# Performance work log

Measured on AMD Instinct MI355X. Metric: run time of the kernel, lower is better.

Reference implementation:

```python
import jax, jax.numpy as jnp
import numpy as np

N_NODES = 15
K = 5
L_IN = 1920
C_OUT = 256
L3 = L_IN - 3 * K + 3  # 1908
EPS = 1e-5


def setup_inputs() -> dict:
    key = jax.random.key(0)
    ks = jax.random.split(key, 18)
    B, E = 128, 56
    s = 0.05
    inp = {
        'X': jax.random.normal(ks[0], (B, N_NODES, L_IN), jnp.float32),
        'edge_index': jax.random.randint(ks[1], (2, E), 0, N_NODES),
        'edge_weight': jax.random.uniform(ks[2], (E,), jnp.float32),
        # grouped conv params (groups = N_NODES): per-group channels 1->16->32->1
        'conv1_w': jax.random.normal(ks[3], (16 * N_NODES, 1, K), jnp.float32) * s,
        'conv1_b': jnp.zeros((16 * N_NODES,), jnp.float32),
        'conv2_w': jax.random.normal(ks[4], (32 * N_NODES, 16, K), jnp.float32) * s,
        'conv2_b': jnp.zeros((32 * N_NODES,), jnp.float32),
        'conv3_w': jax.random.normal(ks[5], (N_NODES, 32, K), jnp.float32) * s,
        'conv3_b': jnp.zeros((N_NODES,), jnp.float32),
        # GCNConv: lin weight [out,in] + bias
        'gcn_w': jax.random.normal(ks[6], (C_OUT, L3), jnp.float32) * s,
        'gcn_b': jnp.zeros((C_OUT,), jnp.float32),
        'lin1_w': jax.random.normal(ks[7], (C_OUT, L_IN), jnp.float32) * s,
        'lin1_b': jnp.zeros((C_OUT,), jnp.float32),
        # GraphNorm params
        'gn_w': jnp.ones((C_OUT,), jnp.float32),
        'gn_b': jnp.zeros((C_OUT,), jnp.float32),
        'gn_ms': jnp.ones((C_OUT,), jnp.float32),
        'out_w': jax.random.normal(ks[8], (16, C_OUT), jnp.float32) * s,
        'out_b': jnp.zeros((16,), jnp.float32),
    }
    return inp


def _gconv(x, w, b):
    # grouped valid conv1d, NCH layout
    y = jax.lax.conv_general_dilated(
        x, w, window_strides=(1,), padding='VALID',
        dimension_numbers=('NCH', 'OIH', 'NCH'),
        feature_group_count=N_NODES)
    return y + b[None, :, None]


def _gcn(x, edge_index, edge_weight, W, b):
    # x: [B, N, L3]; batched GCNConv with shared edge structure (no per-t loop)
    src, dst = edge_index[0], edge_index[1]
    loop = jnp.arange(N_NODES)
    src = jnp.concatenate([src, loop])
    dst = jnp.concatenate([dst, loop])
    ew = jnp.concatenate([edge_weight, jnp.ones((N_NODES,), edge_weight.dtype)])
    deg = jnp.zeros((N_NODES,), ew.dtype).at[dst].add(ew)  # in-degree on target
    dinv = jnp.where(deg > 0, jax.lax.rsqrt(deg), 0.0)
    norm = dinv[src] * ew * dinv[dst]  # [E']
    xl = jnp.einsum('bnf,of->bno', x, W)  # [B, N, C_OUT]
    msg = norm[None, :, None] * xl[:, src, :]  # [B, E', C_OUT]
    out = jnp.zeros_like(xl).at[:, dst, :].add(msg)
    return out + b


def reference(X, edge_index, edge_weight, conv1_w, conv1_b, conv2_w, conv2_b,
              conv3_w, conv3_b, gcn_w, gcn_b, lin1_w, lin1_b, gn_w, gn_b,
              gn_ms, out_w, out_b):
    h = jax.nn.leaky_relu(_gconv(X, conv1_w, conv1_b), 0.01)
    h = jax.nn.leaky_relu(_gconv(h, conv2_w, conv2_b), 0.01)
    h = jax.nn.leaky_relu(_gconv(h, conv3_w, conv3_b), 0.01)  # [B, N, L3]
    T = _gcn(h, edge_index, edge_weight, gcn_w, gcn_b)  # [B, N, C_OUT]
    # GraphNorm with batch=None -> single graph over dim 0
    mean = T.mean(axis=0, keepdims=True)
    out = T - mean * gn_ms
    var = (out * out).mean(axis=0, keepdims=True)
    T = gn_w * out / jnp.sqrt(var + EPS) + gn_b
    T = jax.nn.elu(T + jnp.einsum('bnl,ol->bno', X, lin1_w) + lin1_b)
    output = T.mean(axis=1)  # global_mean_pool over nodes -> [B, C_OUT]
    class_output = output @ out_w.T + out_b  # [B, 16]
    return (output, class_output)
```

## Files before the change

kernel.cpp:

```cpp
#include <hip/hip_runtime.h>

typedef unsigned short u16;
typedef unsigned int   u32;

typedef short shortx8   __attribute__((ext_vector_type(8)));
typedef float floatx4   __attribute__((ext_vector_type(4)));
typedef float floatx16  __attribute__((ext_vector_type(16)));
typedef u32   uintx4    __attribute__((ext_vector_type(4)));

typedef u32     u32a     __attribute__((may_alias));
typedef uintx4  uintx4a  __attribute__((may_alias));
typedef shortx8 shortx8a __attribute__((may_alias));

__device__ __forceinline__ u16 f2bf(float f){
  union { float f; u32 i; } v; v.f = f;
  return (u16)((v.i + 0x7fffu + ((v.i >> 16) & 1u)) >> 16);
}
__device__ __forceinline__ u16 f2bf_fast(float f){
  union { float f; u32 i; } v; v.f = f;
  return (u16)((v.i + 0x8000u) >> 16);
}
__device__ __forceinline__ u32 pack2(float lo, float hi){
  union { float f; u32 i; } a, b; a.f = lo; b.f = hi;
  return __builtin_amdgcn_perm(b.i + 0x8000u, a.i + 0x8000u, 0x07060302u);
}
__device__ __forceinline__ u32 cvtpk2(float lo, float hi){
#if __has_builtin(__builtin_amdgcn_cvt_pk_bf16_f32)
  auto pv = __builtin_amdgcn_cvt_pk_bf16_f32(lo, hi);
  if constexpr (sizeof(pv) == 4){
    u32 out; __builtin_memcpy(&out, &pv, 4); return out;
  } else {
    return pack2(lo, hi);
  }
#else
  return pack2(lo, hi);
#endif
}
__device__ __forceinline__ float lrelu(float v){ return fmaxf(v, 0.01f*v); }

__global__ void __launch_bounds__(256, 4) fused_conv(
    const float* __restrict__ X,
    const float* __restrict__ w1, const float* __restrict__ b1,
    const float* __restrict__ w2, const float* __restrict__ b2,
    const float* __restrict__ w3, const float* __restrict__ b3,
    u16* __restrict__ h3p, u16* __restrict__ Xb,
    const float* __restrict__ lw, u16* __restrict__ lwb,
    const float* __restrict__ gw, u16* __restrict__ gwp){
  const int tid  = threadIdx.x;
  const int node = blockIdx.z;
  const int p0   = blockIdx.x * 120;
  const int b0   = blockIdx.y * 8;

  __shared__ __attribute__((aligned(16))) u16 sH1[2*1632];
  __shared__ __attribute__((aligned(16))) u16 sH2[2*2720];
  __shared__ __attribute__((aligned(16))) u16 sW2f[2560];
  __shared__ __attribute__((aligned(16))) u16 sW3f[160];
  __shared__ u16 sXb[8*136];
  __shared__ float sW1[80], sB1[16], sB2[32];

  {
    const int bid = blockIdx.x + 16*(blockIdx.y + 16*blockIdx.z);
    int gid = bid*256 + tid;
    if (gid < 491520){
      lwb[gid] = f2bf(lw[gid]);
    } else {
      int g2 = gid - 491520;
      int row = g2 / 1920;
      int col = g2 - row*1920;
      gwp[g2] = (col < 1908) ? f2bf(gw[row*1908 + col]) : (u16)0;
    }
  }

  {
    const int bls = tid >> 5, i0 = tid & 31;
    const float* xrow = X  + (size_t)((b0 + bls)*15 + node)*1920;
    u16*        xbrow = Xb + (size_t)((b0 + bls)*15 + node)*1920;
    #pragma unroll
    for (int u = 0; u < 5; ++u){
      int i = i0 + 32*u;
      if (i < 136){
        int g = p0 + i;
        float xv = (g < 1920) ? xrow[g] : 0.f;
        u16 xb = f2bf_fast(xv);
        sXb[bls*136 + i] = xb;
        if (i < 120) xbrow[g] = xb;
      }
    }
    #pragma unroll
    for (int u = 0; u < 10; ++u){
      int d = tid + 256*u;
      int j = d & 7, oc = (d >> 3) & 31, kh = (d >> 8) & 1, tap = d >> 9;
      sW2f[d] = f2bf(w2[node*2560 + (oc*16 + kh*8 + j)*5 + tap]);
    }
    if (tid < 160){
      int icc = tid / 5, tp = tid - 5*icc;
      sW3f[tp*32 + icc] = f2bf(w3[node*160 + tid]);
    }
    if (tid < 80) sW1[tid] = w1[node*80 + tid];
    if (tid < 16) sB1[tid] = b1[node*16 + tid];
    if (tid < 32) sB2[tid] = b2[node*32 + tid];
  }
  __syncthreads();

  const int w = tid >> 6, lane = tid & 63;
  const int pw = w >> 1, ph = w & 1;
  const int m = lane & 15, quad = lane >> 4;
  const int t32 = lane & 31, kh = lane >> 5;

  shortx8 a2t[5];
  #pragma unroll
  for (int tap = 0; tap < 5; ++tap)
    a2t[tap] = *(const shortx8a*)&sW2f[((tap*2 + kh)*32 + t32)*8];

  float biasr[16];
  #pragma unroll
  for (int r = 0; r < 16; ++r)
    biasr[r] = sB2[(r&3) + 8*(r>>2) + 4*kh];

  shortx8 a3[5];
  {
    const shortx8 zv = {0,0,0,0,0,0,0,0};
    #pragma unroll
    for (int tp = 0; tp < 5; ++tp){
      shortx8 t = *(const shortx8a*)&sW3f[tp*32 + quad*8];
      a3[tp] = (m == 0) ? t : zv;
    }
  }
  const float b3v = b3[node];

  u16* h1w = sH1 + pw*1632;
  u16* h2w = sH2 + pw*2720;
  for (int i = lane + ph*64; i < 160; i += 128) h2w[2560 + i] = 0;

  const int c1ic = (lane & 7)*2;
  const int cc   = (lane >> 3) + ph*8;
  const int t0c  = cc*5;
  float wa[5], wb[5];
  #pragma unroll
  for (int k = 0; k < 5; ++k){ wa[k] = sW1[c1ic*5 + k]; wb[k] = sW1[c1ic*5 + 5 + k]; }
  const float ba = sB1[c1ic], bbv = sB1[c1ic + 1];

  for (int bb = 0; bb < 4; ++bb){
    const int bl = pw + bb*2;
    const int rg = (b0 + bl)*15 + node;

    #pragma unroll
    for (int tt = 0; tt < 2; ++tt){
      const int p = p0 + tt*60;

      if (t0c < 68){
        const u16* xr = sXb + bl*136 + tt*60;
        union { u32 i; float f; } cv;
        float xw[5];
        #pragma unroll
        for (int k = 0; k < 4; ++k){ cv.i = ((u32)xr[t0c+k]) << 16; xw[k] = cv.f; }
        #pragma unroll
        for (int i = 0; i < 5; ++i){
          const int t = t0c + i;
          cv.i = ((u32)xr[t + 4]) << 16; xw[4] = cv.f;
          float va = ba  + wa[0]*xw[0] + wa[1]*xw[1] + wa[2]*xw[2] + wa[3]*xw[3] + wa[4]*xw[4];
          float vb = bbv + wb[0]*xw[0] + wb[1]*xw[1] + wb[2]*xw[2] + wb[3]*xw[3] + wb[4]*xw[4];
          va = lrelu(va); vb = lrelu(vb);
          if (t < 68) *(u32a*)(h1w + t*24 + c1ic) = cvtpk2(va, vb);
          xw[0] = xw[1]; xw[1] = xw[2]; xw[2] = xw[3]; xw[3] = xw[4];
        }
      }
      __syncthreads();

      {
        const int t0 = ph*32;
        floatx16 acc;
        #pragma unroll
        for (int r = 0; r < 16; ++r) acc[r] = biasr[r];
        #pragma unroll
        for (int tap = 0; tap < 5; ++tap){
          shortx8 bfr = *(const shortx8a*)(h1w + (t0 + t32 + tap)*24 + kh*8);
          acc = __builtin_amdgcn_mfma_f32_32x32x16_bf16(a2t[tap], bfr, acc, 0, 0, 0);
        }
        u16* dst = h2w + (t0 + t32)*40;
        #pragma unroll
        for (int r = 0; r < 16; r += 2){
          float v0 = lrelu(acc[r]);
          float v1 = lrelu(acc[r+1]);
          const int oc0 = (r&3) + 8*(r>>2) + 4*kh;
          *(u32a*)(dst + oc0) = cvtpk2(v0, v1);
        }
      }
      __syncthreads();

      #pragma unroll
      for (int i = 0; i < 2; ++i){
        const int nt = 2*ph + i;
        floatx4 acc3 = {0.f,0.f,0.f,0.f};
        if (lane < 16) acc3[0] = b3v;
        #pragma unroll
        for (int tp = 0; tp < 5; ++tp){
          shortx8 bfr = *(const shortx8a*)(h2w + (nt*16 + m + tp)*40 + quad*8);
          acc3 = __builtin_amdgcn_mfma_f32_16x16x32_bf16(a3[tp], bfr, acc3, 0, 0, 0);
        }
        const int tl = nt*16 + lane;
        if (lane < 16 && tl < 60){
          const int t3 = p + tl;
          float v = lrelu(acc3[0]);
          h3p[(size_t)rg*1920 + t3] = (t3 < 1908) ? f2bf_fast(v) : (u16)0;
        }
      }
    }
  }
}

__global__ void __launch_bounds__(256) gemm_nt(
    const u16* __restrict__ A0, const u16* __restrict__ B0, float* __restrict__ O0,
    const u16* __restrict__ A1, const u16* __restrict__ B1, float* __restrict__ O1,
    float* __restrict__ gZ){
  const int job = blockIdx.z;
  const u16* A; const u16* Bm; float* O;
  if (job == 0){ A = A0; Bm = B0; O = O0; } else { A = A1; Bm = B1; O = O1; }
  __shared__ __attribute__((aligned(16))) u16 sA[64*88];
  __shared__ __attribute__((aligned(16))) u16 sB[64*88];
  const int tid = threadIdx.x;
  if (blockIdx.x == 0 && blockIdx.y == 0 && job == 0){
    #pragma unroll
    for (int u = 0; u < 30; ++u) gZ[tid + 256*u] = 0.f;
  }
  const int m0 = blockIdx.x*64, n0 = blockIdx.y*64;
  const int row = tid >> 2, kc = tid & 3;
  const int w = tid >> 6, lane = tid & 63;
  const int m = lane & 15, quad = lane >> 4;
  const int mo = (w & 1)*32, no = (w >> 1)*32;
  floatx4 acc[2][2];
  #pragma unroll
  for (int i = 0; i < 2; ++i)
    #pragma unroll
    for (int j = 0; j < 2; ++j)
      #pragma unroll
      for (int r = 0; r < 4; ++r) acc[i][j][r] = 0.f;

  const u16* ap = A  + (size_t)(m0 + row)*1920 + kc*8;
  const u16* bp = Bm + (size_t)(n0 + row)*1920 + kc*8;
  for (int kt = 0; kt < 30; ++kt){
    uintx4 va0 = *(const uintx4a*)ap;
    uintx4 va1 = *(const uintx4a*)(ap + 32);
    uintx4 vb0 = *(const uintx4a*)bp;
    uintx4 vb1 = *(const uintx4a*)(bp + 32);
    ap += 64; bp += 64;
    *(uintx4a*)&sA[row*88 + kc*8]      = va0;
    *(uintx4a*)&sA[row*88 + 32 + kc*8] = va1;
    *(uintx4a*)&sB[row*88 + kc*8]      = vb0;
    *(uintx4a*)&sB[row*88 + 32 + kc*8] = vb1;
    __syncthreads();
    #pragma unroll
    for (int ks = 0; ks < 64; ks += 32){
      const shortx8 af0 = *(const shortx8a*)&sA[(mo      + m)*88 + ks + quad*8];
      const shortx8 af1 = *(const shortx8a*)&sA[(mo + 16 + m)*88 + ks + quad*8];
      const shortx8 bf0 = *(const shortx8a*)&sB[(no      + m)*88 + ks + quad*8];
      const shortx8 bf1 = *(const shortx8a*)&sB[(no + 16 + m)*88 + ks + quad*8];
      acc[0][0] = __builtin_amdgcn_mfma_f32_16x16x32_bf16(af0, bf0, acc[0][0], 0, 0, 0);
      acc[0][1] = __builtin_amdgcn_mfma_f32_16x16x32_bf16(af0, bf1, acc[0][1], 0, 0, 0);
      acc[1][0] = __builtin_amdgcn_mfma_f32_16x16x32_bf16(af1, bf0, acc[1][0], 0, 0, 0);
      acc[1][1] = __builtin_amdgcn_mfma_f32_16x16x32_bf16(af1, bf1, acc[1][1], 0, 0, 0);
    }
    __syncthreads();
  }
  #pragma unroll
  for (int mi = 0; mi < 2; ++mi)
    #pragma unroll
    for (int ni = 0; ni < 2; ++ni)
      #pragma unroll
      for (int r = 0; r < 4; ++r){
        int rr = m0 + mo + mi*16 + quad*4 + r;
        int cc = n0 + no + ni*16 + m;
        O[(size_t)rr*256 + cc] = acc[mi][ni][r];
      }
}

__global__ void __launch_bounds__(256) gcn_agg(
    const float* __restrict__ xl, const int* __restrict__ ei,
    const float* __restrict__ ew, const float* __restrict__ gcn_b,
    float* __restrict__ Tpre, float* __restrict__ gS, float* __restrict__ gS2){
  const int b = blockIdx.x, tid = threadIdx.x;
  __shared__ float sxl[15*256];
  __shared__ float s_deg[15], s_dinv[15], s_norm[71];
  __shared__ int   s_cnt[15], s_start[16], s_fill[15], s_srcl[71];
  if (tid < 15){ s_deg[tid] = 0.f; s_cnt[tid] = 0; s_fill[tid] = 0; }
  #pragma unroll
  for (int n = 0; n < 15; ++n)
    sxl[n*256 + tid] = xl[(size_t)(b*15 + n)*256 + tid];
  __syncthreads();
  int se = 0, de = 0; float we = 0.f;
  if (tid < 71){
    if (tid < 56){ se = ei[tid]; de = ei[56 + tid]; we = ew[tid]; }
    else         { se = tid - 56; de = tid - 56; we = 1.0f; }
    atomicAdd(&s_deg[de], we);
    atomicAdd(&s_cnt[de], 1);
  }
  __syncthreads();
  if (tid < 15) s_dinv[tid] = s_deg[tid] > 0.f ? rsqrtf(s_deg[tid]) : 0.f;
  if (tid == 0){
    int a = 0;
    for (int n = 0; n < 15; ++n){ s_start[n] = a; a += s_cnt[n]; }
    s_start[15] = a;
  }
  __syncthreads();
  if (tid < 71){
    float nrm = s_dinv[se]*we*s_dinv[de];
    int pos = s_start[de] + atomicAdd(&s_fill[de], 1);
    s_srcl[pos] = se; s_norm[pos] = nrm;
  }
  __syncthreads();
  const float gb = gcn_b[tid];
  for (int n = 0; n < 15; ++n){
    float acc = gb;
    const int e0 = s_start[n], e1 = s_start[n+1];
    for (int idx = e0; idx < e1; ++idx)
      acc += s_norm[idx]*sxl[s_srcl[idx]*256 + tid];
    Tpre[(size_t)(b*15 + n)*256 + tid] = acc;
    atomicAdd(&gS [n*256 + tid], acc);
    atomicAdd(&gS2[n*256 + tid], acc*acc);
  }
}

__global__ void __launch_bounds__(256) finalize_k(
    const float* __restrict__ Tpre, const float* __restrict__ l1,
    const float* __restrict__ gS, const float* __restrict__ gS2,
    const float* __restrict__ gn_ms, const float* __restrict__ gn_w,
    const float* __restrict__ gn_b, const float* __restrict__ lin1_b,
    const float* __restrict__ out_w, const float* __restrict__ out_b,
    float* __restrict__ dout){
  const int b = blockIdx.x, tid = threadIdx.x;
  __shared__ float spool[256], spart[256];
  const float gnb = gn_b[tid], lb = lin1_b[tid];
  const float gms = gn_ms[tid], gwc = gn_w[tid];
  float acc = 0.f;
  #pragma unroll
  for (int n = 0; n < 15; ++n){
    const float s  = gS [n*256 + tid];
    const float s2 = gS2[n*256 + tid];
    const float mean = s*(1.f/128.f);
    const float mo   = mean*gms;
    float var = s2*(1.f/128.f) - 2.f*mo*mean + mo*mo;
    var = fmaxf(var, 0.f);
    const float scal = gwc*rsqrtf(var + 1e-5f);
    float t = (Tpre[(size_t)(b*15 + n)*256 + tid] - mo)*scal
              + gnb + l1[(size_t)(b*15 + n)*256 + tid] + lb;
    t = t > 0.f ? t : (__expf(t) - 1.f);
    acc += t;
  }
  const float pool = acc*(1.f/15.f);
  dout[b*256 + tid] = pool;
  spool[tid] = pool;
  __syncthreads();
  const int j = tid >> 4, q = tid & 15;
  float s = 0.f;
  for (int i = 0; i < 16; ++i){
    int cc = q + i*16;
    s += spool[cc]*out_w[j*256 + cc];
  }
  spart[tid] = s;
  __syncthreads();
  if (tid < 16){
    float tot = out_b[tid];
    #pragma unroll
    for (int i = 0; i < 16; ++i) tot += spart[tid*16 + i];
    dout[32768 + b*16 + tid] = tot;
  }
}

extern "C" void kernel_launch(void* const* d_in, const int* in_sizes, int n_in,
                              void* d_out, int out_size, void* d_ws, size_t ws_size,
                              hipStream_t stream){
  (void)in_sizes; (void)n_in; (void)out_size; (void)ws_size;
  const float* X    = (const float*)d_in[0];
  const int*   ei   = (const int*)d_in[1];
  const float* ew   = (const float*)d_in[2];
  const float* w1   = (const float*)d_in[3];
  const float* b1   = (const float*)d_in[4];
  const float* w2   = (const float*)d_in[5];
  const float* b2   = (const float*)d_in[6];
  const float* w3   = (const float*)d_in[7];
  const float* b3   = (const float*)d_in[8];
  const float* gw   = (const float*)d_in[9];
  const float* gb   = (const float*)d_in[10];
  const float* lw   = (const float*)d_in[11];
  const float* lb   = (const float*)d_in[12];
  const float* gnw  = (const float*)d_in[13];
  const float* gnb  = (const float*)d_in[14];
  const float* gnms = (const float*)d_in[15];
  const float* ow   = (const float*)d_in[16];
  const float* ob   = (const float*)d_in[17];

  char* ws = (char*)d_ws;
  u16*   h3p  = (u16*)(ws + 0);
  u16*   gwp  = (u16*)(ws + 7372800);
  u16*   Xb   = (u16*)(ws + 8355840);
  u16*   lwb  = (u16*)(ws + 15728640);
  float* xl   = (float*)(ws + 16711680);
  float* l1   = (float*)(ws + 18677760);
  float* gS   = (float*)(ws + 20643840);
  float* gS2  = (float*)(ws + 20659200);
  float* Tpre = (float*)(ws + 0);

  fused_conv<<<dim3(16, 16, 15), dim3(256), 0, stream>>>(X, w1, b1, w2, b2, w3, b3,
                                                         h3p, Xb, lw, lwb, gw, gwp);
  gemm_nt   <<<dim3(30, 4, 2),   dim3(256), 0, stream>>>(Xb, lwb, l1, h3p, gwp, xl, gS);
  gcn_agg   <<<dim3(128),        dim3(256), 0, stream>>>(xl, ei, ew, gb, Tpre, gS, gS2);
  finalize_k<<<dim3(128),        dim3(256), 0, stream>>>(Tpre, l1, gS, gS2,
                                                         gnms, gnw, gnb, lb, ow, ob,
                                                         (float*)d_out);
}
```

Baseline: 197.9 us.

## Compute conv1 with split-bf16 MFMA from a pre-staged im2col window

Replaces the scalar FMA-based first grouped convolution with a 16x16x32 bf16 MFMA, using a hi/lo bf16 split of the conv1 weights to keep accuracy. Each batch row first builds an im2col-style window of shifted input values in shared memory (stored in spare slots of the merged h1/h2 buffer), and an extra barrier is added per batch row. H1 and H2 shared buffers are merged into one paired array so the staging can reuse their padding area. The aim is to cut VALU work in conv1. The cost is the extra barrier, two MFMAs per tile, wasted lanes (only quad 0 supplies data) and more complex indexing.

Result: no change. 199.2 us (+0.7%).

```diff
diff --git a/kernel.cpp b/kernel.cpp
--- a/kernel.cpp
+++ b/kernel.cpp
@@ -6,9 +6,11 @@
 typedef short shortx8   __attribute__((ext_vector_type(8)));
 typedef float floatx4   __attribute__((ext_vector_type(4)));
 typedef float floatx16  __attribute__((ext_vector_type(16)));
+typedef u32   uintx2    __attribute__((ext_vector_type(2)));
 typedef u32   uintx4    __attribute__((ext_vector_type(4)));
 
 typedef u32     u32a     __attribute__((may_alias));
+typedef uintx2  uintx2a  __attribute__((may_alias));
 typedef uintx4  uintx4a  __attribute__((may_alias));
 typedef shortx8 shortx8a __attribute__((may_alias));
 
@@ -51,11 +53,10 @@
   const int p0   = blockIdx.x * 120;
   const int b0   = blockIdx.y * 8;
 
-  __shared__ __attribute__((aligned(16))) u16 sH1[2*1632];
-  __shared__ __attribute__((aligned(16))) u16 sH2[2*2720];
+  __shared__ __attribute__((aligned(16))) u16 sPair[2][4352];
   __shared__ __attribute__((aligned(16))) u16 sW2f[2560];
   __shared__ __attribute__((aligned(16))) u16 sW3f[160];
-  __shared__ u16 sXb[8*136];
+  __shared__ __attribute__((aligned(16))) u16 sXb[8*136];
   __shared__ float sW1[80], sB1[16], sB2[32];
 
   {
@@ -99,6 +100,10 @@
     if (tid < 80) sW1[tid] = w1[node*80 + tid];
     if (tid < 16) sB1[tid] = b1[node*16 + tid];
     if (tid < 32) sB2[tid] = b2[node*32 + tid];
+    {
+      const int pr = tid >> 7, idx = tid & 127;
+      sPair[pr][1632 + (64 + (idx >> 5))*40 + (idx & 31)] = 0;
+    }
   }
   __syncthreads();
 
@@ -128,41 +133,76 @@
   }
   const float b3v = b3[node];
 
-  u16* h1w = sH1 + pw*1632;
-  u16* h2w = sH2 + pw*2720;
-  for (int i = lane + ph*64; i < 160; i += 128) h2w[2560 + i] = 0;
-
-  const int c1ic = (lane & 7)*2;
-  const int cc   = (lane >> 3) + ph*8;
-  const int t0c  = cc*5;
-  float wa[5], wb[5];
-  #pragma unroll
-  for (int k = 0; k < 5; ++k){ wa[k] = sW1[c1ic*5 + k]; wb[k] = sW1[c1ic*5 + 5 + k]; }
-  const float ba = sB1[c1ic], bbv = sB1[c1ic + 1];
+  shortx8 a1h = {0,0,0,0,0,0,0,0}, a1l = {0,0,0,0,0,0,0,0};
+  if (quad == 0){
+    const float* wrow = sW1 + m*5;
+    #pragma unroll
+    for (int j = 0; j < 5; ++j){
+      float wv = wrow[j];
+      u16 h = f2bf(wv);
+      union { u32 i; float f; } hf; hf.i = ((u32)h) << 16;
+      u16 l = f2bf(wv - hf.f);
+      a1h[j] = (short)h; a1l[j] = (short)l;
+    }
+  }
+  float biasA[4];
+  #pragma unroll
+  for (int r = 0; r < 4; ++r) biasA[r] = sB1[quad*4 + r];
+
+  u16* h1w = sPair[pw];
+  u16* h2w = sPair[pw] + 1632;
 
   for (int bb = 0; bb < 4; ++bb){
     const int bl = pw + bb*2;
     const int rg = (b0 + bl)*15 + node;
 
+    {
+      const int s = tid & 127;
+      if (s < 68){
+        const u32* xb32 = (const u32*)sXb + bl*68;
+        u32 r0 = xb32[s];
+        u32 r1 = (s+1 < 68) ? xb32[s+1] : 0u;
+        u32 r2 = (s+2 < 68) ? xb32[s+2] : 0u;
+        u32 r3 = (s+3 < 68) ? xb32[s+3] : 0u;
+        u32 r4 = (s+4 < 68) ? xb32[s+4] : 0u;
+        const int te = 2*s, to = 2*s + 1;
+        const int offE = (s < 34) ? te*24 + 16 : 1632 + (te - 68)*40 + 32;
+        const int offO = (s < 34) ? to*24 + 16 : 1632 + (to - 68)*40 + 32;
+        uintx4 ve = {r0, r1, r2, r3};
+        uintx4 vo = {__builtin_amdgcn_alignbit(r1, r0, 16),
+                     __builtin_amdgcn_alignbit(r2, r1, 16),
+                     __builtin_amdgcn_alignbit(r3, r2, 16),
+                     __builtin_amdgcn_alignbit(r4, r3, 16)};
+        *(uintx4a*)(h1w + offE) = ve;
+        *(uintx4a*)(h1w + offO) = vo;
+      }
+    }
+    __syncthreads();
+
     #pragma unroll
     for (int tt = 0; tt < 2; ++tt){
       const int p = p0 + tt*60;
 
-      if (t0c < 68){
-        const u16* xr = sXb + bl*136 + tt*60;
-        union { u32 i; float f; } cv;
-        float xw[5];
-        #pragma unroll
-        for (int k = 0; k < 4; ++k){ cv.i = ((u32)xr[t0c+k]) << 16; xw[k] = cv.f; }
-        #pragma unroll
-        for (int i = 0; i < 5; ++i){
-          const int t = t0c + i;
-          cv.i = ((u32)xr[t + 4]) << 16; xw[4] = cv.f;
-          float va = ba  + wa[0]*xw[0] + wa[1]*xw[1] + wa[2]*xw[2] + wa[3]*xw[3] + wa[4]*xw[4];
-          float vb = bbv + wb[0]*xw[0] + wb[1]*xw[1] + wb[2]*xw[2] + wb[3]*xw[3] + wb[4]*xw[4];
-          va = lrelu(va); vb = lrelu(vb);
-          if (t < 68) *(u32a*)(h1w + t*24 + c1ic) = cvtpk2(va, vb);
-          xw[0] = xw[1]; xw[1] = xw[2]; xw[2] = xw[3]; xw[3] = xw[4];
+      #pragma unroll
+      for (int ti = 0; ti < 3; ++ti){
+        const int T = ph + 2*ti;
+        if (T < 5){
+          const int tr = T*16 + m;
+          int row = tt*60 + tr;
+          row = row > 135 ? 135 : row;
+          shortx8 bfr = {0,0,0,0,0,0,0,0};
+          if (quad == 0){
+            const int off = (row < 68) ? row*24 + 16 : 1632 + (row - 68)*40 + 32;
+            bfr = *(const shortx8a*)(h1w + off);
+          }
+          floatx4 acc = {biasA[0], biasA[1], biasA[2], biasA[3]};
+          acc = __builtin_amdgcn_mfma_f32_16x16x32_bf16(a1l, bfr, acc, 0, 0, 0);
+          acc = __builtin_amdgcn_mfma_f32_16x16x32_bf16(a1h, bfr, acc, 0, 0, 0);
+          if (tr < 68){
+            uintx2 pk = { cvtpk2(lrelu(acc[0]), lrelu(acc[1])),
+                          cvtpk2(lrelu(acc[2]), lrelu(acc[3])) };
+            *(uintx2a*)(h1w + tr*24 + quad*4) = pk;
+          }
         }
       }
       __syncthreads();
```
